# Performance work log

Hardware: AMD Instinct MI355X
Metric: run time of the kernel (lower is better)

The kernel has to match this reference:

```python
import jax, jax.numpy as jnp
import numpy as np

N, C, H, W = 8, 256, 64, 64
NW = 8            # n_win (regions per side)
TOPK = 4
HEADS = 16
MLP = 4 * C
SCALE = C ** -0.5  # qk_dim = dim in BiLevelRoutingAttention


def _ln(x, g, b, eps=1e-6):
    mu = x.mean(-1, keepdims=True)
    var = ((x - mu) ** 2).mean(-1, keepdims=True)
    return (x - mu) * jax.lax.rsqrt(var + eps) * g + b


def setup_inputs() -> dict:
    key = jax.random.key(0)
    ks = jax.random.split(key, 8)
    f = lambda k, shp: jax.random.normal(k, shp, jnp.float32) * 0.02
    return {
        "x": jax.random.normal(ks[0], (N, C, H, W), jnp.float32),
        "norm1_g": jnp.ones((C,), jnp.float32), "norm1_b": jnp.zeros((C,), jnp.float32),
        "qkv_w": f(ks[1], (C, 3 * C)), "qkv_b": jnp.zeros((3 * C,), jnp.float32),
        "lepe_w": f(ks[2], (5, 5, 1, C)), "lepe_b": jnp.zeros((C,), jnp.float32),
        "gamma1": -jnp.ones((C,), jnp.float32), "gamma2": -jnp.ones((C,), jnp.float32),
        "norm2_g": jnp.ones((C,), jnp.float32), "norm2_b": jnp.zeros((C,), jnp.float32),
        "mlp_w1": f(ks[3], (C, MLP)), "mlp_b1": jnp.zeros((MLP,), jnp.float32),
        "mlp_w2": f(ks[4], (MLP, C)), "mlp_b2": jnp.zeros((C,), jnp.float32),
    }


def _bra(x, qkv_w, qkv_b, lepe_w, lepe_b):
    # BiLevelRoutingAttention: x is NHWC
    n, hh, ww, c = x.shape
    h, w = hh // NW, ww // NW
    P, hw = NW * NW, h * w
    qkv = x @ qkv_w + qkv_b                    # [n,H,W,3c]
    q, k, v = qkv[..., :c], qkv[..., c:2 * c], qkv[..., 2 * c:]

    def win(t):                                 # [n,H,W,d] -> [n,P,h,w,d]
        d = t.shape[-1]
        return t.reshape(n, NW, h, NW, w, d).transpose(0, 1, 3, 2, 4, 5).reshape(n, P, h, w, d)

    qw, kw, vw = win(q), win(k), win(v)
    q_pix = qw.reshape(n, P, hw, c)
    k_pix = kw.reshape(n, P, hw, c)
    v_pix = vw.reshape(n, P, hw, c)

    # region-level routing (q/k detached; routing weights unused since mul_weight='none')
    q_win = jax.lax.stop_gradient(qw.mean((2, 3)))   # [n,P,c]
    k_win = jax.lax.stop_gradient(kw.mean((2, 3)))
    logit = jnp.einsum('npc,nqc->npq', q_win * SCALE, k_win)
    _, idx = jax.lax.top_k(logit, TOPK)              # [n,P,TOPK]

    gather = jax.vmap(lambda t, i: t[i])             # over batch
    k_sel = gather(k_pix, idx)                       # [n,P,TOPK,hw,c]
    v_sel = gather(v_pix, idx)

    dh = c // HEADS
    # channel layout is (m c): split heads on last dim
    qh = q_pix.reshape(n, P, hw, HEADS, dh).transpose(0, 1, 3, 2, 4)                       # [n,P,m,hw,dh]
    kh = k_sel.reshape(n, P, TOPK, hw, HEADS, dh).transpose(0, 1, 4, 2, 3, 5).reshape(n, P, HEADS, TOPK * hw, dh)
    vh = v_sel.reshape(n, P, TOPK, hw, HEADS, dh).transpose(0, 1, 4, 2, 3, 5).reshape(n, P, HEADS, TOPK * hw, dh)

    attn = jax.nn.softmax(jnp.einsum('npmqd,npmkd->npmqk', qh * SCALE, kh), axis=-1)
    out = jnp.einsum('npmqk,npmkd->npmqd', attn, vh)                                       # [n,P,m,hw,dh]
    out = out.transpose(0, 1, 3, 2, 4).reshape(n, P, hw, c)
    out = out.reshape(n, NW, NW, h, w, c).transpose(0, 1, 3, 2, 4, 5).reshape(n, hh, ww, c)

    # lepe: 5x5 depthwise conv over full-image v (side_dwconv=5)
    lepe = jax.lax.conv_general_dilated(
        v, lepe_w, (1, 1), 'SAME',
        dimension_numbers=('NHWC', 'HWIO', 'NHWC'),
        feature_group_count=c) + lepe_b
    return out + lepe   # wo = Identity for param_attention='qkv'


def reference(x, norm1_g, norm1_b, qkv_w, qkv_b, lepe_w, lepe_b, gamma1, gamma2,
              norm2_g, norm2_b, mlp_w1, mlp_b1, mlp_w2, mlp_b2):
    xp = x.transpose(0, 2, 3, 1)  # NCHW -> NHWC
    xp = xp + gamma1 * _bra(_ln(xp, norm1_g, norm1_b), qkv_w, qkv_b, lepe_w, lepe_b)
    z = _ln(xp, norm2_g, norm2_b)
    m = jax.nn.gelu(z @ mlp_w1 + mlp_b1, approximate=False) @ mlp_w2 + mlp_b2
    xp = xp + gamma2 * m
    return xp.transpose(0, 3, 1, 2)  # NHWC -> NCHW
```

## Files before the change

### kernel.cpp

```cpp
#include <hip/hip_runtime.h>

typedef unsigned short u16;
typedef __bf16 bf16x8 __attribute__((ext_vector_type(8)));
typedef short s16x4 __attribute__((ext_vector_type(4)));
typedef float f32x4 __attribute__((ext_vector_type(4)));

#define SCALE_ATT 0.0625f

static __device__ __forceinline__ u16 f2b(float f) {
    __bf16 h = (__bf16)f;
    union { __bf16 b; u16 u; } v; v.b = h;
    return v.u;
}
static __device__ __forceinline__ float b2f(u16 h) {
    union { unsigned u; float f; } v; v.u = ((unsigned)h) << 16;
    return v.f;
}

#if defined(__has_builtin)
#if __has_builtin(__builtin_amdgcn_mfma_f32_16x16x16bf16_1k)
#define HAVE_MFMA16 1
#endif
#if __has_builtin(__builtin_amdgcn_exp2f)
#define EXP2(x) __builtin_amdgcn_exp2f(x)
#endif
#if __has_builtin(__builtin_amdgcn_rcpf)
#define RCP(x) __builtin_amdgcn_rcpf(x)
#endif
#if __has_builtin(__builtin_amdgcn_global_load_lds)
#define HAVE_GLOADLDS 1
#endif
#endif
#ifndef EXP2
#define EXP2(x) exp2f(x)
#endif
#ifndef RCP
#define RCP(x) (1.0f / (x))
#endif

static __device__ __forceinline__ f32x4 mfma16(s16x4 a, s16x4 b, f32x4 c) {
#ifdef HAVE_MFMA16
    return __builtin_amdgcn_mfma_f32_16x16x16bf16_1k(a, b, c, 0, 0, 0);
#else
    f32x4 d;
    asm volatile("v_mfma_f32_16x16x16_bf16 %0, %1, %2, %3\n\ts_nop 7\n\ts_nop 7"
                 : "=v"(d) : "v"(a), "v"(b), "v"(c));
    return d;
#endif
}

#ifdef HAVE_GLOADLDS
static __device__ __forceinline__ void gload16(const u16* g, u16* l) {
    __builtin_amdgcn_global_load_lds(
        (const __attribute__((address_space(1))) void*)g,
        (__attribute__((address_space(3))) void*)l, 16, 0, 0);
}
#endif

static __device__ __forceinline__ float gelu_fast(float v) {
    float v2 = v * v;
    float w = fmaf(v2, 0.044715f, 1.0f);
    float arg = v * w * 2.30211754f;
    float e = EXP2(arg);
    float r = RCP(e + 1.0f);
    return fmaf(-v, r, v);
}

__global__ void wtrans_kernel(const float* __restrict__ src, u16* __restrict__ dst,
                              int R, int C) {
    int i = blockIdx.x * 256 + threadIdx.x;
    if (i >= R * C) return;
    int r = i / C, c = i % C;
    dst[(size_t)c * R + r] = f2b(src[i]);
}

__global__ __launch_bounds__(256) void ln_xpose_kernel(
    const float* __restrict__ x, const float* __restrict__ g, const float* __restrict__ b,
    float* __restrict__ xp, u16* __restrict__ ln1, float* __restrict__ pool_part) {
    __shared__ float xs[256][65];
    __shared__ float ps[4][64], ps2[4][64];
    __shared__ float mvmu[64], mvrs[64];
    int nb = blockIdx.x; int n = nb >> 6, y = nb & 63;
    int t = threadIdx.x;
    const float4* src = (const float4*)(x + ((size_t)(n * 256 + t) * 64 + y) * 64);
    for (int x4 = 0; x4 < 16; ++x4) {
        float4 v = src[x4];
        xs[t][x4 * 4 + 0] = v.x; xs[t][x4 * 4 + 1] = v.y;
        xs[t][x4 * 4 + 2] = v.z; xs[t][x4 * 4 + 3] = v.w;
    }
    __syncthreads();
    int part = t >> 6, l = t & 63;
    float s1 = 0.f, s2 = 0.f;
    for (int c = 0; c < 64; ++c) { float v = xs[part * 64 + c][l]; s1 += v; s2 += v * v; }
    ps[part][l] = s1; ps2[part][l] = s2;
    __syncthreads();
    if (t < 64) {
        float su = ps[0][t] + ps[1][t] + ps[2][t] + ps[3][t];
        float sq = ps2[0][t] + ps2[1][t] + ps2[2][t] + ps2[3][t];
        float mu = su * (1.f / 256.f);
        float var = sq * (1.f / 256.f) - mu * mu;
        mvmu[t] = mu; mvrs[t] = rsqrtf(var + 1e-6f);
    }
    __syncthreads();
    float gc = g[t], bc = b[t];
    size_t tokbase = (size_t)nb * 64;
    float pw = 0.f;
    for (int xx = 0; xx < 64; ++xx) {
        float raw = xs[t][xx];
        float val = (raw - mvmu[xx]) * mvrs[xx] * gc + bc;
        size_t tok = tokbase + xx;
        xp[tok * 256 + t] = raw;
        ln1[tok * 256 + t] = f2b(val);
        pw += val;
        if ((xx & 7) == 7) {
            pool_part[((size_t)nb * 8 + (xx >> 3)) * 256 + t] = pw;
            pw = 0.f;
        }
    }
}

__global__ void pool_reduce_kernel(const float* __restrict__ pool_part,
                                   float* __restrict__ pooled) {
    int nb = blockIdx.x; int n = nb >> 6, p = nb & 63;
    int wi = p >> 3, wj = p & 7;
    int t = threadIdx.x;
    float s = 0.f;
    for (int r = 0; r < 8; ++r)
        s += pool_part[((size_t)((n * 64 + wi * 8 + r) * 8 + wj)) * 256 + t];
    pooled[(size_t)nb * 256 + t] = s * (1.f / 64.f);
}

__global__ void qkwin_kernel(const float* __restrict__ pooled,
                             const float* __restrict__ qkv_w, const float* __restrict__ qkv_b,
                             float* __restrict__ qk_win) {
    __shared__ float pr[256];
    int nb = blockIdx.x; int t = threadIdx.x;
    pr[t] = pooled[(size_t)nb * 256 + t];
    __syncthreads();
    float aq = qkv_b[t], ak = qkv_b[256 + t];
    for (int k = 0; k < 256; ++k) {
        float pv = pr[k];
        aq += pv * qkv_w[(size_t)k * 768 + t];
        ak += pv * qkv_w[(size_t)k * 768 + 256 + t];
    }
    qk_win[(size_t)nb * 512 + t] = aq;
    qk_win[(size_t)nb * 512 + 256 + t] = ak;
}

__global__ void routing_kernel(const float* __restrict__ qk_win, int* __restrict__ idxp) {
    __shared__ float lg_[64];
    int nb = blockIdx.x; int n = nb >> 6;
    int t = threadIdx.x;
    const float* qw = qk_win + (size_t)nb * 512;
    const float* kw = qk_win + (size_t)(n * 64 + t) * 512 + 256;
    float s = 0.f;
    for (int c = 0; c < 256; ++c) s += qw[c] * kw[c];
    lg_[t] = s * SCALE_ATT;
    __syncthreads();
    if (t == 0) {
        for (int j = 0; j < 4; ++j) {
            float best = -INFINITY; int bi = 0;
            for (int q = 0; q < 64; ++q) if (lg_[q] > best) { best = lg_[q]; bi = q; }
            idxp[nb * 4 + j] = bi;
            lg_[bi] = -INFINITY;
        }
    }
}

template <int EPI>
__global__ __launch_bounds__(256) void gemm_kernel(
    const u16* __restrict__ A, const u16* __restrict__ Bt,
    const float* __restrict__ bias, u16* __restrict__ outb,
    int M, int Nn, int K,
    const float* __restrict__ resid_in, const float* __restrict__ gamma,
    float* __restrict__ resid_out) {
    __shared__ u16 As[8192];
    __shared__ u16 Bs[8192];
    int t = threadIdx.x;
    int rowBase = blockIdx.x * 128, colBase = blockIdx.y * 128;
    int wid = t >> 6, lane = t & 63;
    int wr = (wid >> 1) * 64, wc = (wid & 1) * 64;
    int lr = lane & 15, g = lane >> 4;
    f32x4 acc[4][4] = {};

    int rA0 = wid * 32 + (lane >> 2);
    int rA1 = rA0 + 16;
    int cs0 = (lane & 3) ^ ((rA0 >> 1) & 3);
    int cs1 = (lane & 3) ^ ((rA1 >> 1) & 3);
    const u16* gA0 = A + (size_t)(rowBase + rA0) * K + cs0 * 8;
    const u16* gA1 = A + (size_t)(rowBase + rA1) * K + cs1 * 8;
    const u16* gB0 = Bt + (size_t)(colBase + rA0) * K + cs0 * 8;
    const u16* gB1 = Bt + (size_t)(colBase + rA1) * K + cs1 * 8;
    u16* lA0 = &As[(wid * 2 + 0) * 512];
    u16* lA1 = &As[(wid * 2 + 1) * 512];
    u16* lB0 = &Bs[(wid * 2 + 0) * 512];
    u16* lB1 = &Bs[(wid * 2 + 1) * 512];

    int cSwz = (g * 16) ^ (((lr >> 1) & 3) << 4);
    const int NT = K >> 5;

#ifdef HAVE_GLOADLDS
    gload16(gA0, lA0);
    gload16(gA1, lA1);
    gload16(gB0, lB0);
    gload16(gB1, lB1);
    int cur = 0;
    for (int tk = 0; tk < NT; ++tk) {
        if (tk + 1 < NT) {
            int koff = (tk + 1) << 5;
            int bo = (cur ^ 1) << 12;
            gload16(gA0 + koff, lA0 + bo);
            gload16(gA1 + koff, lA1 + bo);
            gload16(gB0 + koff, lB0 + bo);
            gload16(gB1 + koff, lB1 + bo);
            asm volatile("s_waitcnt vmcnt(4)" ::: "memory");
        } else {
            asm volatile("s_waitcnt vmcnt(0)" ::: "memory");
        }
        __builtin_amdgcn_s_barrier();
        asm volatile("" ::: "memory");
        const char* pAc = (const char*)As + (cur << 13);
        const char* pBc = (const char*)Bs + (cur << 13);
        bf16x8 af[4], bfr[4];
        #pragma unroll
        for (int m = 0; m < 4; ++m)
            af[m] = *(const bf16x8*)(pAc + (wr + m * 16 + lr) * 64 + cSwz);
        #pragma unroll
        for (int nn = 0; nn < 4; ++nn)
            bfr[nn] = *(const bf16x8*)(pBc + (wc + nn * 16 + lr) * 64 + cSwz);
        #pragma unroll
        for (int m = 0; m < 4; ++m)
            #pragma unroll
            for (int nn = 0; nn < 4; ++nn)
                acc[m][nn] = __builtin_amdgcn_mfma_f32_16x16x32_bf16(af[m], bfr[nn], acc[m][nn], 0, 0, 0);
        asm volatile("" ::: "memory");
        __builtin_amdgcn_s_barrier();
        cur ^= 1;
    }
#else
    const char* pAc = (const char*)As;
    const char* pBc = (const char*)Bs;
    for (int tk = 0; tk < NT; ++tk) {
        int koff = tk << 5;
        float4 a0 = *(const float4*)(gA0 + koff);
        float4 a1 = *(const float4*)(gA1 + koff);
        float4 b0 = *(const float4*)(gB0 + koff);
        float4 b1 = *(const float4*)(gB1 + koff);
        __syncthreads();
        *(float4*)&lA0[lane * 8] = a0;
        *(float4*)&lA1[lane * 8] = a1;
        *(float4*)&lB0[lane * 8] = b0;
        *(float4*)&lB1[lane * 8] = b1;
        __syncthreads();
        bf16x8 af[4], bfr[4];
        #pragma unroll
        for (int m = 0; m < 4; ++m)
            af[m] = *(const bf16x8*)(pAc + (wr + m * 16 + lr) * 64 + cSwz);
        #pragma unroll
        for (int nn = 0; nn < 4; ++nn)
            bfr[nn] = *(const bf16x8*)(pBc + (wc + nn * 16 + lr) * 64 + cSwz);
        #pragma unroll
        for (int m = 0; m < 4; ++m)
            #pragma unroll
            for (int nn = 0; nn < 4; ++nn)
                acc[m][nn] = __builtin_amdgcn_mfma_f32_16x16x32_bf16(af[m], bfr[nn], acc[m][nn], 0, 0, 0);
        __syncthreads();
    }
#endif
    #pragma unroll
    for (int m = 0; m < 4; ++m)
        #pragma unroll
        for (int nn = 0; nn < 4; ++nn) {
            int col = colBase + wc + nn * 16 + lr;
            float bcol = bias[col];
            #pragma unroll
            for (int r = 0; r < 4; ++r) {
                int row = rowBase + wr + m * 16 + g * 4 + r;
                float v = acc[m][nn][r] + bcol;
                if constexpr (EPI == 0) {
                    outb[(size_t)row * Nn + col] = f2b(v);
                } else if constexpr (EPI == 1) {
                    outb[(size_t)row * Nn + col] = f2b(gelu_fast(v));
                } else {
                    float yv = resid_in[(size_t)row * 256 + col] + gamma[col] * v;
                    resid_out[(size_t)row * 256 + col] = yv;
                }
            }
        }
}

__global__ __launch_bounds__(256) void lepe_kernel(
    const u16* __restrict__ qkv, const float* __restrict__ w,
    const float* __restrict__ bias, u16* __restrict__ lepe) {
    __shared__ u16 vt[5][64][64];
    int nb = blockIdx.x, cg = blockIdx.y;
    int n = nb >> 6, y = nb & 63;
    int t = threadIdx.x;
    {
        int xs = t >> 3, cs = t & 7;
        #pragma unroll
        for (int r = 0; r < 5; ++r) {
            int yy = y - 2 + r;
            bool ok = (yy >= 0 && yy <= 63);
            #pragma unroll
            for (int half = 0; half < 2; ++half) {
                int x = xs + half * 32;
                float4 v = {0.f, 0.f, 0.f, 0.f};
                if (ok)
                    v = *(const float4*)(qkv +
                        ((size_t)((n * 64 + yy) * 64 + x)) * 768 + 512 + cg * 64 + cs * 8);
                *(float4*)&vt[r][x][cs * 8] = v;
            }
        }
    }
    __syncthreads();
    int c = t & 63, x0 = (t >> 6) * 16;
    float wv[25];
    #pragma unroll
    for (int i = 0; i < 25; ++i) wv[i] = w[i * 256 + cg * 64 + c];
    float bc = bias[cg * 64 + c];
    float win[5][5];
    #pragma unroll
    for (int r = 0; r < 5; ++r)
        #pragma unroll
        for (int j = 0; j < 4; ++j) {
            int x2 = x0 - 2 + j;
            win[r][j] = (x2 >= 0) ? b2f(vt[r][x2][c]) : 0.f;
        }
    #pragma unroll
    for (int xi = 0; xi < 16; ++xi) {
        int xx = x0 + xi;
        int xl = xx + 2;
        #pragma unroll
        for (int r = 0; r < 5; ++r)
            win[r][4] = (xl <= 63) ? b2f(vt[r][xl][c]) : 0.f;
        float s = bc;
        #pragma unroll
        for (int r = 0; r < 5; ++r)
            #pragma unroll
            for (int j = 0; j < 5; ++j)
                s = fmaf(wv[r * 5 + j], win[r][j], s);
        lepe[((size_t)nb * 64 + xx) * 256 + cg * 64 + c] = f2b(s);
        #pragma unroll
        for (int r = 0; r < 5; ++r)
            #pragma unroll
            for (int j = 0; j < 4; ++j)
                win[r][j] = win[r][j + 1];
    }
}

__global__ __launch_bounds__(512) void attn_kernel(
    const u16* __restrict__ qkv, const int* __restrict__ idxp,
    u16* __restrict__ attn_out) {
    __shared__ __align__(16) char smem_[39424];
    u16 (*qs)[36]   = (u16 (*)[36])smem_;
    u16 (*ks)[36]   = (u16 (*)[36])(smem_ + 4608);
    u16 (*vts)[256] = (u16 (*)[256])(smem_ + 23040);
    float (*os)[36] = (float (*)[36])(smem_ + 4608);
    int nb = blockIdx.x, hg = blockIdx.y;
    int n = nb >> 6, p = nb & 63;
    int y0 = (p >> 3) * 8, x0 = (p & 7) * 8;
    int t = threadIdx.x;
    int w0 = idxp[nb * 4 + 0], w1 = idxp[nb * 4 + 1];
    int w2 = idxp[nb * 4 + 2], w3 = idxp[nb * 4 + 3];
    {
        int tok = t >> 3, seg = t & 7;
        int tokg = (n * 64 + y0 + (tok >> 3)) * 64 + x0 + (tok & 7);
        *(uint2*)&qs[tok][seg * 4] =
            *(const uint2*)(qkv + (size_t)tokg * 768 + hg * 32 + seg * 4);
    }
    {
        int key = t & 255, half = t >> 8;
        int ws = (key >> 6) == 0 ? w0 : (key >> 6) == 1 ? w1 : (key >> 6) == 2 ? w2 : w3;
        int kp = key & 63;
        int tokk = (n * 64 + (ws >> 3) * 8 + (kp >> 3)) * 64 + (ws & 7) * 8 + (kp & 7);
        const u16* kbase = qkv + (size_t)tokk * 768 + 256 + hg * 32 + half * 16;
        *(uint2*)&ks[key][half * 16 + 0]  = *(const uint2*)(kbase + 0);
        *(uint2*)&ks[key][half * 16 + 4]  = *(const uint2*)(kbase + 4);
        *(uint2*)&ks[key][half * 16 + 8]  = *(const uint2*)(kbase + 8);
        *(uint2*)&ks[key][half * 16 + 12] = *(const uint2*)(kbase + 12);
        const u16* vbase = kbase + 256;
        union { float4 f[2]; u16 u[16]; } vu;
        vu.f[0] = *(const float4*)vbase;
        vu.f[1] = *(const float4*)(vbase + 8);
        #pragma unroll
        for (int c2 = 0; c2 < 16; ++c2)
            vts[half * 16 + c2][key ^ (c2 << 2)] = vu.u[c2];
    }
    __syncthreads();

    int wid = t >> 6, lane = t & 63, lr = lane & 15, g = lane >> 4;
    int hh = wid & 1, q0 = (wid >> 1) * 16, c0 = hh * 16;
    f32x4 zf4 = {0.f, 0.f, 0.f, 0.f};
    s16x4 qf = *(const s16x4*)&qs[q0 + lr][c0 + g * 4];
    f32x4 sacc[16];
    __builtin_amdgcn_s_setprio(1);
    #pragma unroll
    for (int kt = 0; kt < 16; ++kt) {
        s16x4 kf = *(const s16x4*)&ks[kt * 16 + lr][c0 + g * 4];
        sacc[kt] = mfma16(kf, qf, zf4);
    }
    __builtin_amdgcn_s_setprio(0);
    float mx = fmaxf(fmaxf(sacc[0][0], sacc[0][1]), fmaxf(sacc[0][2], sacc[0][3]));
    #pragma unroll
    for (int kt = 1; kt < 16; ++kt) {
        mx = fmaxf(mx, fmaxf(sacc[kt][0], sacc[kt][1]));
        mx = fmaxf(mx, fmaxf(sacc[kt][2], sacc[kt][3]));
    }
    mx = fmaxf(mx, __shfl_xor(mx, 16, 64));
    mx = fmaxf(mx, __shfl_xor(mx, 32, 64));
    const float k1 = 0.09016844005556021f;
    float negmk = -mx * k1;
    float dsum = 0.f;
    s16x4 pf[16];
    #pragma unroll
    for (int kt = 0; kt < 16; ++kt) {
        float e0 = EXP2(fmaf(sacc[kt][0], k1, negmk));
        float e1 = EXP2(fmaf(sacc[kt][1], k1, negmk));
        float e2 = EXP2(fmaf(sacc[kt][2], k1, negmk));
        float e3 = EXP2(fmaf(sacc[kt][3], k1, negmk));
        dsum += (e0 + e1) + (e2 + e3);
        union { unsigned u[2]; s16x4 s; } pk;
        asm("v_cvt_pk_bf16_f32 %0, %1, %2" : "=v"(pk.u[0]) : "v"(e0), "v"(e1));
        asm("v_cvt_pk_bf16_f32 %0, %1, %2" : "=v"(pk.u[1]) : "v"(e2), "v"(e3));
        pf[kt] = pk.s;
    }
    dsum += __shfl_xor(dsum, 16, 64);
    dsum += __shfl_xor(dsum, 32, 64);
    float rden = 1.f / dsum;
    __syncthreads();
    f32x4 o0 = zf4, o1 = zf4;
    __builtin_amdgcn_s_setprio(1);
    #pragma unroll
    for (int kt = 0; kt < 16; kt += 2) {
        s16x4 v0 = *(const s16x4*)&vts[c0 + lr][(kt * 16 + g * 4) ^ (lr << 2)];
        o0 = mfma16(v0, pf[kt], o0);
        s16x4 v1 = *(const s16x4*)&vts[c0 + lr][((kt + 1) * 16 + g * 4) ^ (lr << 2)];
        o1 = mfma16(v1, pf[kt + 1], o1);
    }
    __builtin_amdgcn_s_setprio(0);
    #pragma unroll
    for (int r = 0; r < 4; ++r)
        os[q0 + lr][c0 + g * 4 + r] = (o0[r] + o1[r]) * rden;
    __syncthreads();
    {
        int tok = t >> 3, cs = (t & 7) * 4;
        int tokg = (n * 64 + y0 + (tok >> 3)) * 64 + x0 + (tok & 7);
        float f0 = os[tok][cs + 0], f1 = os[tok][cs + 1];
        float f2 = os[tok][cs + 2], f3 = os[tok][cs + 3];
        uint2 pk;
        asm("v_cvt_pk_bf16_f32 %0, %1, %2" : "=v"(pk.x) : "v"(f0), "v"(f1));
        asm("v_cvt_pk_bf16_f32 %0, %1, %2" : "=v"(pk.y) : "v"(f2), "v"(f3));
        *(uint2*)(attn_out + (size_t)tokg * 256 + hg * 32 + cs) = pk;
    }
}

__global__ __launch_bounds__(256) void resid1_ln2_kernel(
    const float* __restrict__ xp, const u16* __restrict__ attn,
    const u16* __restrict__ lepe, const float* __restrict__ g1,
    const float* __restrict__ n2g, const float* __restrict__ n2b,
    float* __restrict__ xp1, u16* __restrict__ z) {
    __shared__ float w1s[4], w2s[4];
    size_t tok = blockIdx.x;
    int t = threadIdx.x;
    float x1 = xp[tok * 256 + t] + g1[t] * (b2f(attn[tok * 256 + t]) + b2f(lepe[tok * 256 + t]));
    xp1[tok * 256 + t] = x1;
    float s1 = x1, s2 = x1 * x1;
    for (int off = 1; off < 64; off <<= 1) {
        s1 += __shfl_xor(s1, off, 64);
        s2 += __shfl_xor(s2, off, 64);
    }
    int wid = t >> 6;
    if ((t & 63) == 0) { w1s[wid] = s1; w2s[wid] = s2; }
    __syncthreads();
    s1 = w1s[0] + w1s[1] + w1s[2] + w1s[3];
    s2 = w2s[0] + w2s[1] + w2s[2] + w2s[3];
    float mu = s1 * (1.f / 256.f);
    float var = s2 * (1.f / 256.f) - mu * mu;
    float rs = rsqrtf(var + 1e-6f);
    z[tok * 256 + t] = f2b((x1 - mu) * rs * n2g[t] + n2b[t]);
}

__global__ __launch_bounds__(256) void out_xpose_kernel(
    const float* __restrict__ yout, float* __restrict__ outp) {
    __shared__ float ys[256][65];
    int nb = blockIdx.x; int n = nb >> 6, y = nb & 63;
    int t = threadIdx.x;
    for (int xx = 0; xx < 64; ++xx)
        ys[t][xx] = yout[((size_t)nb * 64 + xx) * 256 + t];
    __syncthreads();
    float4* dst = (float4*)(outp + ((size_t)(n * 256 + t) * 64 + y) * 64);
    for (int x4 = 0; x4 < 16; ++x4) {
        float4 v = { ys[t][x4 * 4 + 0], ys[t][x4 * 4 + 1],
                     ys[t][x4 * 4 + 2], ys[t][x4 * 4 + 3] };
        dst[x4] = v;
    }
}

extern "C" void kernel_launch(void* const* d_in, const int* in_sizes, int n_in,
                              void* d_out, int out_size, void* d_ws, size_t ws_size,
                              hipStream_t stream) {
    (void)in_sizes; (void)n_in; (void)out_size; (void)ws_size;
    const float* x      = (const float*)d_in[0];
    const float* n1g    = (const float*)d_in[1];
    const float* n1b    = (const float*)d_in[2];
    const float* qkv_w  = (const float*)d_in[3];
    const float* qkv_b  = (const float*)d_in[4];
    const float* lepe_w = (const float*)d_in[5];
    const float* lepe_b = (const float*)d_in[6];
    const float* g1     = (const float*)d_in[7];
    const float* g2     = (const float*)d_in[8];
    const float* n2g    = (const float*)d_in[9];
    const float* n2b    = (const float*)d_in[10];
    const float* w1     = (const float*)d_in[11];
    const float* b1     = (const float*)d_in[12];
    const float* w2     = (const float*)d_in[13];
    const float* b2     = (const float*)d_in[14];
    float* outp = (float*)d_out;
    char* ws = (char*)d_ws;

    float* xp        = (float*)(ws + 0);
    u16*   ln1       = (u16*)(ws + 33554432);
    u16*   qkv       = (u16*)(ws + 50331648);
    u16*   attn_b    = (u16*)(ws + 100663296);
    u16*   lepe      = (u16*)(ws + 134217728);
    u16*   zbuf      = (u16*)(ws + 150994944);
    float* pool_part = (float*)(ws + 167772160);
    float* pooled    = (float*)(ws + 171966464);
    float* qk_win    = (float*)(ws + 172490752);
    int*   idxb      = (int*)(ws + 173539328);
    u16*   wt_qkv    = (u16*)(ws + 173547520);
    u16*   wt_m1     = (u16*)(ws + 173940736);
    u16*   wt_m2     = (u16*)(ws + 174465024);
    u16*   hbuf      = ln1;
    float* xp1       = outp;
    float* yout      = (float*)(ws + 100663296);

    wtrans_kernel<<<768, 256, 0, stream>>>(qkv_w, wt_qkv, 256, 768);
    wtrans_kernel<<<1024, 256, 0, stream>>>(w1, wt_m1, 256, 1024);
    wtrans_kernel<<<1024, 256, 0, stream>>>(w2, wt_m2, 1024, 256);

    ln_xpose_kernel<<<512, 256, 0, stream>>>(x, n1g, n1b, xp, ln1, pool_part);
    pool_reduce_kernel<<<512, 256, 0, stream>>>(pool_part, pooled);
    qkwin_kernel<<<512, 256, 0, stream>>>(pooled, qkv_w, qkv_b, qk_win);
    routing_kernel<<<512, 64, 0, stream>>>(qk_win, idxb);

    gemm_kernel<0><<<dim3(256, 6), 256, 0, stream>>>(
        ln1, wt_qkv, qkv_b, qkv, 32768, 768, 256, nullptr, nullptr, nullptr);

    lepe_kernel<<<dim3(512, 4), 256, 0, stream>>>(qkv, lepe_w, lepe_b, lepe);
    attn_kernel<<<dim3(512, 8), 512, 0, stream>>>(qkv, idxb, attn_b);

    resid1_ln2_kernel<<<32768, 256, 0, stream>>>(xp, attn_b, lepe, g1, n2g, n2b, xp1, zbuf);

    gemm_kernel<1><<<dim3(256, 8), 256, 0, stream>>>(
        zbuf, wt_m1, b1, hbuf, 32768, 1024, 256, nullptr, nullptr, nullptr);
    gemm_kernel<2><<<dim3(256, 2), 256, 0, stream>>>(
        hbuf, wt_m2, b2, nullptr, 32768, 256, 1024, xp1, g2, yout);

    out_xpose_kernel<<<512, 256, 0, stream>>>(yout, outp);
}
```

Before: 266.7 us.

## Store residuals in bf16, fuse output transpose into MLP2 epilogue, warp-per-token LN2

The residual stream xp and xp1 is now stored as bf16 instead of fp32, which halves that traffic. The final NHWC->NCHW transpose is folded into the second MLP GEMM epilogue, which stages the tile through swizzled shared memory and writes NCHW directly, so the separate out_xpose kernel and the yout buffer are gone. resid1_ln2 now processes one token per wavefront with vectorized loads, which removes block-level syncs. The cost is precision loss from rounding the residual to bf16 and extra syncs in the GEMM epilogue.

New measurement: 238.7 us. 1.12x faster.

```diff
diff --git a/kernel.cpp b/kernel.cpp
--- a/kernel.cpp
+++ b/kernel.cpp
@@ -76,7 +76,7 @@
 
 __global__ __launch_bounds__(256) void ln_xpose_kernel(
     const float* __restrict__ x, const float* __restrict__ g, const float* __restrict__ b,
-    float* __restrict__ xp, u16* __restrict__ ln1, float* __restrict__ pool_part) {
+    u16* __restrict__ xp, u16* __restrict__ ln1, float* __restrict__ pool_part) {
     __shared__ float xs[256][65];
     __shared__ float ps[4][64], ps2[4][64];
     __shared__ float mvmu[64], mvrs[64];
@@ -109,7 +109,7 @@
         float raw = xs[t][xx];
         float val = (raw - mvmu[xx]) * mvrs[xx] * gc + bc;
         size_t tok = tokbase + xx;
-        xp[tok * 256 + t] = raw;
+        xp[tok * 256 + t] = f2b(raw);
         ln1[tok * 256 + t] = f2b(val);
         pw += val;
         if ((xx & 7) == 7) {
@@ -172,10 +172,11 @@
     const u16* __restrict__ A, const u16* __restrict__ Bt,
     const float* __restrict__ bias, u16* __restrict__ outb,
     int M, int Nn, int K,
-    const float* __restrict__ resid_in, const float* __restrict__ gamma,
+    const u16* __restrict__ resid_in, const float* __restrict__ gamma,
     float* __restrict__ resid_out) {
-    __shared__ u16 As[8192];
-    __shared__ u16 Bs[8192];
+    __shared__ u16 smem[16384];
+    u16* As = smem;
+    u16* Bs = smem + 8192;
     int t = threadIdx.x;
     int rowBase = blockIdx.x * 128, colBase = blockIdx.y * 128;
     int wid = t >> 6, lane = t & 63;
@@ -267,26 +268,63 @@
         __syncthreads();
     }
 #endif
-    #pragma unroll
-    for (int m = 0; m < 4; ++m)
-        #pragma unroll
-        for (int nn = 0; nn < 4; ++nn) {
-            int col = colBase + wc + nn * 16 + lr;
-            float bcol = bias[col];
+    if constexpr (EPI == 2) {
+        int n = rowBase >> 12;
+        int y0 = (rowBase >> 6) & 63;
+        float* ts = (float*)smem;
+        #pragma unroll
+        for (int half = 0; half < 2; ++half) {
+            if ((wid & 1) == half) {
+                #pragma unroll
+                for (int m = 0; m < 4; ++m)
+                    #pragma unroll
+                    for (int nn = 0; nn < 4; ++nn) {
+                        int colL = nn * 16 + lr;
+                        int col = colBase + half * 64 + colL;
+                        float bcol = bias[col];
+                        float gcol = gamma[col];
+                        int s = ((colL & 7) << 2) | ((colL >> 3) & 1);
+                        #pragma unroll
+                        for (int r = 0; r < 4; ++r) {
+                            int rowIdx = wr + m * 16 + g * 4 + r;
+                            float v = acc[m][nn][r] + bcol;
+                            float yv = b2f(resid_in[(size_t)(rowBase + rowIdx) * 256 + col]) + gcol * v;
+                            ts[colL * 128 + (rowIdx ^ s)] = yv;
+                        }
+                    }
+            }
+            __syncthreads();
             #pragma unroll
-            for (int r = 0; r < 4; ++r) {
-                int row = rowBase + wr + m * 16 + g * 4 + r;
-                float v = acc[m][nn][r] + bcol;
-                if constexpr (EPI == 0) {
-                    outb[(size_t)row * Nn + col] = f2b(v);
-                } else if constexpr (EPI == 1) {
-                    outb[(size_t)row * Nn + col] = f2b(gelu_fast(v));
-                } else {
-                    float yv = resid_in[(size_t)row * 256 + col] + gamma[col] * v;
-                    resid_out[(size_t)row * 256 + col] = yv;
+            for (int j = 0; j < 16; ++j) {
+                int ch = wid * 16 + j;
+                int s = ((ch & 7) << 2) | ((ch >> 3) & 1);
+                float v0 = ts[ch * 128 + (lane ^ s)];
+                float v1 = ts[ch * 128 + ((64 + lane) ^ s)];
+                float* gb = resid_out + ((size_t)(n * 256 + colBase + half * 64 + ch) * 64 + y0) * 64;
+                gb[lane] = v0;
+                gb[64 + lane] = v1;
+            }
+            __syncthreads();
+        }
+    } else {
+        #pragma unroll
+        for (int m = 0; m < 4; ++m)
+            #pragma unroll
+            for (int nn = 0; nn < 4; ++nn) {
+                int col = colBase + wc + nn * 16 + lr;
+                float bcol = bias[col];
+                #pragma unroll
+                for (int r = 0; r < 4; ++r) {
+                    int row = rowBase + wr + m * 16 + g * 4 + r;
+                    float v = acc[m][nn][r] + bcol;
+                    if constexpr (EPI == 0) {
+                        outb[(size_t)row * Nn + col] = f2b(v);
+                    } else {
+                        outb[(size_t)row * Nn + col] = f2b(gelu_fast(v));
+                    }
                 }
             }
-        }
+    }
 }
 
 __global__ __launch_bounds__(256) void lepe_kernel(
@@ -456,45 +494,49 @@
 }
 
 __global__ __launch_bounds__(256) void resid1_ln2_kernel(
-    const float* __restrict__ xp, const u16* __restrict__ attn,
+    const u16* __restrict__ xp, const u16* __restrict__ attn,
     const u16* __restrict__ lepe, const float* __restrict__ g1,
     const float* __restrict__ n2g, const float* __restrict__ n2b,
-    float* __restrict__ xp1, u16* __restrict__ z) {
-    __shared__ float w1s[4], w2s[4];
-    size_t tok = blockIdx.x;
+    u16* __restrict__ xp1, u16* __restrict__ z) {
     int t = threadIdx.x;
-    float x1 = xp[tok * 256 + t] + g1[t] * (b2f(attn[tok * 256 + t]) + b2f(lepe[tok * 256 + t]));
-    xp1[tok * 256 + t] = x1;
-    float s1 = x1, s2 = x1 * x1;
+    int wid = t >> 6, lane = t & 63;
+    size_t tok = (size_t)blockIdx.x * 4 + wid;
+    size_t base = tok * 256 + lane * 4;
+    uint2 xv = *(const uint2*)(xp + base);
+    uint2 av = *(const uint2*)(attn + base);
+    uint2 lv = *(const uint2*)(lepe + base);
+    float4 g1v = *(const float4*)(g1 + lane * 4);
+    float4 ngv = *(const float4*)(n2g + lane * 4);
+    float4 nbv = *(const float4*)(n2b + lane * 4);
+    const u16* xu = (const u16*)&xv;
+    const u16* au = (const u16*)&av;
+    const u16* lu = (const u16*)&lv;
+    const float* g1f = (const float*)&g1v;
+    const float* ngf = (const float*)&ngv;
+    const float* nbf = (const float*)&nbv;
+    float x1[4];
+    float s1 = 0.f, s2 = 0.f;
+    #pragma unroll
+    for (int j = 0; j < 4; ++j) {
+        float xx = b2f(xu[j]) + g1f[j] * (b2f(au[j]) + b2f(lu[j]));
+        x1[j] = xx; s1 += xx; s2 += xx * xx;
+    }
+    #pragma unroll
     for (int off = 1; off < 64; off <<= 1) {
         s1 += __shfl_xor(s1, off, 64);
         s2 += __shfl_xor(s2, off, 64);
     }
-    int wid = t >> 6;
-    if ((t & 63) == 0) { w1s[wid] = s1; w2s[wid] = s2; }
-    __syncthreads();
-    s1 = w1s[0] + w1s[1] + w1s[2] + w1s[3];
-    s2 = w2s[0] + w2s[1] + w2s[2] + w2s[3];
     float mu = s1 * (1.f / 256.f);
     float var = s2 * (1.f / 256.f) - mu * mu;
     float rs = rsqrtf(var + 1e-6f);
-    z[tok * 256 + t] = f2b((x1 - mu) * rs * n2g[t] + n2b[t]);
-}
-
-__global__ __launch_bounds__(256) void out_xpose_kernel(
-    const float* __restrict__ yout, float* __restrict__ outp) {
-    __shared__ float ys[256][65];
-    int nb = blockIdx.x; int n = nb >> 6, y = nb & 63;
-    int t = threadIdx.x;
-    for (int xx = 0; xx < 64; ++xx)
-        ys[t][xx] = yout[((size_t)nb * 64 + xx) * 256 + t];
-    __syncthreads();
-    float4* dst = (float4*)(outp + ((size_t)(n * 256 + t) * 64 + y) * 64);
-    for (int x4 = 0; x4 < 16; ++x4) {
-        float4 v = { ys[t][x4 * 4 + 0], ys[t][x4 * 4 + 1],
-                     ys[t][x4 * 4 + 2], ys[t][x4 * 4 + 3] };
-        dst[x4] = v;
-    }
+    u16 zo[4], xo[4];
+    #pragma unroll
+    for (int j = 0; j < 4; ++j) {
+        zo[j] = f2b((x1[j] - mu) * rs * ngf[j] + nbf[j]);
+        xo[j] = f2b(x1[j]);
+    }
+    *(uint2*)(z + base) = *(uint2*)zo;
+    *(uint2*)(xp1 + base) = *(uint2*)xo;
 }
 
 extern "C" void kernel_launch(void* const* d_in, const int* in_sizes, int n_in,
@@ -519,7 +561,7 @@
     float* outp = (float*)d_out;
     char* ws = (char*)d_ws;
 
-    float* xp        = (float*)(ws + 0);
+    u16*   xp_b      = (u16*)(ws + 0);
     u16*   ln1       = (u16*)(ws + 33554432);
     u16*   qkv       = (u16*)(ws + 50331648);
     u16*   attn_b    = (u16*)(ws + 100663296);
@@ -533,14 +575,12 @@
     u16*   wt_m1     = (u16*)(ws + 173940736);
     u16*   wt_m2     = (u16*)(ws + 174465024);
     u16*   hbuf      = ln1;
-    float* xp1       = outp;
-    float* yout      = (float*)(ws + 100663296);
 
     wtrans_kernel<<<768, 256, 0, stream>>>(qkv_w, wt_qkv, 256, 768);
     wtrans_kernel<<<1024, 256, 0, stream>>>(w1, wt_m1, 256, 1024);
     wtrans_kernel<<<1024, 256, 0, stream>>>(w2, wt_m2, 1024, 256);
 
-    ln_xpose_kernel<<<512, 256, 0, stream>>>(x, n1g, n1b, xp, ln1, pool_part);
+    ln_xpose_kernel<<<512, 256, 0, stream>>>(x, n1g, n1b, xp_b, ln1, pool_part);
     pool_reduce_kernel<<<512, 256, 0, stream>>>(pool_part, pooled);
     qkwin_kernel<<<512, 256, 0, stream>>>(pooled, qkv_w, qkv_b, qk_win);
     routing_kernel<<<512, 64, 0, stream>>>(qk_win, idxb);
@@ -551,12 +591,10 @@
     lepe_kernel<<<dim3(512, 4), 256, 0, stream>>>(qkv, lepe_w, lepe_b, lepe);
     attn_kernel<<<dim3(512, 8), 512, 0, stream>>>(qkv, idxb, attn_b);
 
-    resid1_ln2_kernel<<<32768, 256, 0, stream>>>(xp, attn_b, lepe, g1, n2g, n2b, xp1, zbuf);
+    resid1_ln2_kernel<<<8192, 256, 0, stream>>>(xp_b, attn_b, lepe, g1, n2g, n2b, xp_b, zbuf);
 
     gemm_kernel<1><<<dim3(256, 8), 256, 0, stream>>>(
         zbuf, wt_m1, b1, hbuf, 32768, 1024, 256, nullptr, nullptr, nullptr);
     gemm_kernel<2><<<dim3(256, 2), 256, 0, stream>>>(
-        hbuf, wt_m2, b2, nullptr, 32768, 256, 1024, xp1, g2, yout);
-
-    out_xpose_kernel<<<512, 256, 0, stream>>>(yout, outp);
-}
+        hbuf, wt_m2, b2, nullptr, 32768, 256, 1024, xp_b, g2, outp);
+}
```
